# Kernel tuning notes

Hardware: AMD Instinct MI355X
Metric: run time of the kernel (lower is better)

## Reference

```python
import jax, jax.numpy as jnp
import numpy as np
import math

B, QL, KL, D, H, FF = 2, 2048, 2048, 512, 8, 2048
DH = D // H

def layernorm(x, g, b, eps=1e-5):
    m = jnp.mean(x, axis=-1, keepdims=True)
    v = jnp.mean((x - m) ** 2, axis=-1, keepdims=True)
    return (x - m) * jax.lax.rsqrt(v + eps) * g + b

def mha(x, mask, wq, bq, wk, bk, wv, bv, wo, bo, kv=None):
    # faithful port of MultiHeadAttention.forward (eval mode, dropout off)
    bs, qlen, dim = x.shape
    src = x if kv is None else kv
    def split(t):
        return t.reshape(bs, -1, H, DH).transpose(0, 2, 1, 3)  # [b,h,l,dh]
    q = split(x @ wq + bq) * (1.0 / math.sqrt(DH))
    k = split(src @ wk + bk)
    v = split(src @ wv + bv)
    scores = jnp.einsum('bhqd,bhkd->bhqk', q, k)
    m = mask[:, None, :, :] if mask.ndim == 3 else mask[:, None, None, :]
    scores = jnp.where(m == 0, -jnp.inf, scores)
    w = jax.nn.softmax(scores.astype(jnp.float32), axis=-1).astype(scores.dtype)
    ctx = jnp.einsum('bhqk,bhkd->bhqd', w, v)
    ctx = ctx.transpose(0, 2, 1, 3).reshape(bs, qlen, dim)
    return ctx @ wo + bo

def decoder_layer(tgt, memory, pos, tkpm, causal_mask, mem_mask,
                  sa, ca, l1w, l1b, l2w, l2b, n1g, n1b, n2g, n2b, n3g, n3b):
    tgt = tgt + pos
    t2 = layernorm(tgt, n1g, n1b)
    t2 = t2 * tkpm[:, :, None]
    t2 = mha(t2, causal_mask, *sa)
    tgt = tgt + t2
    t2 = layernorm(tgt, n2g, n2b)
    t2 = mha(t2, mem_mask, *ca, kv=memory)
    tgt = tgt + t2
    t2 = layernorm(tgt, n3g, n3b)
    t2 = jax.nn.relu(t2 @ l1w + l1b) @ l2w + l2b
    tgt = tgt + t2
    tgt = tgt * tkpm[:, :, None]
    return tgt

def setup_inputs() -> dict:
    key = jax.random.key(0)
    ks = jax.random.split(key, 32)
    it = iter(list(ks))
    def nrm(shape, s=0.02):
        return jax.random.normal(next(it), shape, jnp.float32) * s
    inp = {}
    inp['cfg'] = 0
    inp['tgt'] = jax.random.normal(next(it), (B, QL, D), jnp.float32)
    inp['memory'] = jax.random.normal(next(it), (B, KL, D), jnp.float32)
    inp['pos'] = jax.random.normal(next(it), (B, QL, D), jnp.float32)
    inp['causal_mask'] = jnp.broadcast_to(jnp.tril(jnp.ones((QL, QL), jnp.int32)), (B, QL, QL))
    inp['tgt_key_padding_mask'] = jnp.ones((B, QL), jnp.float32)
    mkpm = jax.random.randint(next(it), (B, KL), 0, 2).astype(jnp.int32)
    inp['memory_key_padding_mask'] = mkpm.at[:, 0].set(1)  # avoid fully-masked rows
    for p in ['sa', 'ca']:
        for w in ['q', 'k', 'v', 'o']:
            inp[f'{p}_{w}_w'] = nrm((D, D))
            inp[f'{p}_{w}_b'] = jnp.zeros((D,), jnp.float32)
    inp['lin1_w'] = nrm((D, FF)); inp['lin1_b'] = jnp.zeros((FF,), jnp.float32)
    inp['lin2_w'] = nrm((FF, D)); inp['lin2_b'] = jnp.zeros((D,), jnp.float32)
    for n in ['n1', 'n2', 'n3']:
        inp[f'{n}_g'] = jnp.ones((D,), jnp.float32)
        inp[f'{n}_b'] = jnp.zeros((D,), jnp.float32)
    return inp

def reference(cfg, tgt, memory, pos, causal_mask, tgt_key_padding_mask, memory_key_padding_mask,
              sa_q_w, sa_q_b, sa_k_w, sa_k_b, sa_v_w, sa_v_b, sa_o_w, sa_o_b,
              ca_q_w, ca_q_b, ca_k_w, ca_k_b, ca_v_w, ca_v_b, ca_o_w, ca_o_b,
              lin1_w, lin1_b, lin2_w, lin2_b,
              n1_g, n1_b, n2_g, n2_b, n3_g, n3_b):
    sa = (sa_q_w, sa_q_b, sa_k_w, sa_k_b, sa_v_w, sa_v_b, sa_o_w, sa_o_b)
    ca = (ca_q_w, ca_q_b, ca_k_w, ca_k_b, ca_v_w, ca_v_b, ca_o_w, ca_o_b)
    return decoder_layer(tgt, memory, pos, tgt_key_padding_mask, causal_mask, memory_key_padding_mask,
                         sa, ca, lin1_w, lin1_b, lin2_w, lin2_b, n1_g, n1_b, n2_g, n2_b, n3_g, n3_b)
```

## Files before the change

kernel.cpp:

```cpp
#include <hip/hip_runtime.h>
#include <hip/hip_bf16.h>
#include <stdint.h>

#define QL   2048
#define KLn  2048
#define DIM  512
#define NH   8
#define DH   64
#define NB   2
#define MROWS (NB*QL)
#define FFD  2048

typedef unsigned short u16;
typedef unsigned int u32;
typedef __attribute__((ext_vector_type(8))) short short8;
typedef __attribute__((ext_vector_type(4))) float f32x4;

__device__ __forceinline__ u16 f2b(float f){
  union { float f; u32 i; } v; v.f = f;
  u32 r = v.i + 0x7FFFu + ((v.i >> 16) & 1u);
  return (u16)(r >> 16);
}
__device__ __forceinline__ float b2f(u16 u){
  union { u32 i; float f; } v; v.i = ((u32)u) << 16; return v.f;
}
__device__ __forceinline__ u32 cvtpk(float a, float b){
  u32 r;
  asm("v_cvt_pk_bf16_f32 %0, %1, %2" : "=v"(r) : "v"(a), "v"(b));
  return r;
}

typedef __attribute__((address_space(3))) void as3void;
typedef __attribute__((address_space(1))) void as1void;
__device__ __forceinline__ void gload_lds16(const void* g, void* l){
  __builtin_amdgcn_global_load_lds((as1void*)g, (as3void*)l, 16, 0, 0);
}

#define BK 64
enum { EPI_BIAS=0, EPI_SCALEQ=1, EPI_RELU=2, EPI_RES=3, EPI_FIN=5, EPI_QKV=6, EPI_KV=7 };
#define QSCALE 0.1803368801111244f

template<int EPI>
__global__ __launch_bounds__(256, 4)
void gemm64(const u16* __restrict__ A, const u16* __restrict__ Bt,
            const float* __restrict__ bias,
            u16* __restrict__ Obf, float* __restrict__ Ores,
            const float* __restrict__ tk, float* __restrict__ fout,
            int K, int N)
{
  __shared__ __align__(16) u16 As[2][64*BK];
  __shared__ __align__(16) u16 Bs[2][64*BK];
  const int t  = threadIdx.x;
  const int l  = t & 63;
  const int lq = l & 15, lg = l >> 4;
  const int w  = t >> 6;
  const int wm = (w >> 1) * 32;
  const int wn = (w & 1) * 32;

  const int gx   = gridDim.x;
  const int nwg  = gx * gridDim.y;
  const int orig = blockIdx.x + gx * blockIdx.y;
  const int wgid = (orig & 7) * (nwg >> 3) + (orig >> 3);
  const int m0 = (wgid / gx) * 64;
  const int n0 = (wgid % gx) * 64;

  const int srow = t >> 3;
  const int scs  = t & 7;

  auto stageG = [&](u16* dA, u16* dB, int k0){
    _Pragma("unroll")
    for (int i = 0; i < 2; ++i){
      const int row = i*32 + srow;
      gload_lds16(A  + (size_t)(m0 + row)*K + k0 + ((scs ^ (row & 7)) << 3),
                  dA + row*BK + scs*8);
      gload_lds16(Bt + (size_t)(n0 + row)*K + k0 + ((scs ^ (row & 7)) << 3),
                  dB + row*BK + scs*8);
    }
  };

  int aoff[2][2], boff[2][2];
  _Pragma("unroll")
  for (int i = 0; i < 2; ++i)
    _Pragma("unroll")
    for (int kc = 0; kc < 2; ++kc){
      const int sw = (((kc*4 + lg) ^ (lq & 7)) << 3);
      aoff[i][kc] = ((wm + i*16 + lq)*BK + sw) * 2;
      boff[i][kc] = ((wn + i*16 + lq)*BK + sw) * 2;
    }

  f32x4 acc[2][2];
  _Pragma("unroll")
  for (int i=0;i<2;i++)
    _Pragma("unroll")
    for (int j=0;j<2;j++) acc[i][j] = (f32x4){0.f,0.f,0.f,0.f};

#define GBODY(BUF, KK)                                                        \
  {                                                                           \
    { const int ks = ((KK) + BK < K) ? (KK) + BK : 0;                         \
      stageG(As[(BUF)^1], Bs[(BUF)^1], ks); }                                 \
    asm volatile("s_waitcnt vmcnt(4)" ::: "memory");                          \
    __builtin_amdgcn_s_barrier();                                             \
    __builtin_amdgcn_sched_barrier(0);                                        \
    short8 af[2][2], bf[2][2];                                                \
    _Pragma("unroll")                                                         \
    for (int kc = 0; kc < 2; ++kc)                                            \
      _Pragma("unroll")                                                       \
      for (int i = 0; i < 2; ++i){                                            \
        af[i][kc] = *(const short8*)((const char*)As + (BUF)*8192 + aoff[i][kc]); \
        bf[i][kc] = *(const short8*)((const char*)Bs + (BUF)*8192 + boff[i][kc]); \
      }                                                                       \
    __builtin_amdgcn_s_barrier();                                             \
    __builtin_amdgcn_s_setprio(1);                                            \
    _Pragma("unroll")                                                         \
    for (int kc = 0; kc < 2; ++kc)                                            \
      _Pragma("unroll")                                                       \
      for (int i = 0; i < 2; ++i)                                             \
        _Pragma("unroll")                                                     \
        for (int j = 0; j < 2; ++j)                                           \
          acc[i][j] = __builtin_amdgcn_mfma_f32_16x16x32_bf16(af[i][kc], bf[j][kc], acc[i][j], 0,0,0); \
    __builtin_amdgcn_s_setprio(0);                                            \
  }

  stageG(As[0], Bs[0], 0);
  for (int k0 = 0; k0 < K; k0 += 2*BK){
    GBODY(0, k0)
    GBODY(1, k0 + BK)
  }
#undef GBODY

  _Pragma("unroll")
  for (int i=0;i<2;i++){
    _Pragma("unroll")
    for (int j=0;j<2;j++){
      _Pragma("unroll")
      for (int rr=0;rr<4;rr++){
        const int row = m0 + wm + i*16 + lg*4 + rr;
        const int col = n0 + wn + j*16 + lq;
        float v = acc[i][j][rr] + bias[col];
        if (EPI == EPI_SCALEQ) v *= QSCALE;
        if (EPI == EPI_RELU)   v = fmaxf(v, 0.f);
        if (EPI == EPI_RES)    Ores[(size_t)row*N + col] += v;
        else if (EPI == EPI_FIN){
          const size_t idx = (size_t)row*N + col;
          fout[idx] = (Ores[idx] + v) * tk[row];
        }
        else if (EPI == EPI_QKV){
          const int seg = col >> 9, c = col & 511;
          if (seg == 0)      Obf[(size_t)row*512 + c] = f2b(v * QSCALE);
          else if (seg == 1){
            const int bb = row >> 11, kv = row & 2047;
            const int hh = c >> 6,  dh = c & 63;
            Obf[(2u<<20) + ((((size_t)(bb*NH + hh) << 11) + kv) << 6) + (dh ^ ((kv & 7) << 3))] = f2b(v);
          }
          else               Obf[(4u<<20) + (size_t)row*512 + c] = f2b(v);
        }
        else if (EPI == EPI_KV){
          const int seg = col >> 9, c = col & 511;
          if (seg == 0){
            const int bb = row >> 11, kv = row & 2047;
            const int hh = c >> 6,  dh = c & 63;
            Obf[((((size_t)(bb*NH + hh) << 11) + kv) << 6) + (dh ^ ((kv & 7) << 3))] = f2b(v);
          }
          else               Obf[(2u<<20) + (size_t)row*512 + c] = f2b(v);
        }
        else                   Obf[(size_t)row*N + col] = f2b(v);
      }
    }
  }
}

template<bool CAUSAL>
__global__ __launch_bounds__(256, 4)
void attn7(const u16* __restrict__ Q, const u16* __restrict__ Kbh,
           const u16* __restrict__ Vth, const float* __restrict__ bias,
           u16* __restrict__ ctxp, float2* __restrict__ mlb)
{
  __shared__ __align__(16) u16 Kl[2][64*64];
  __shared__ __align__(16) u16 Vl[2][64*64];
  const int tid = threadIdx.x;
  const int l  = tid & 63;
  const int w  = tid >> 6;
  const int lq = l & 15, lg = l >> 4;
  const int h    = blockIdx.y;
  const int b    = blockIdx.z >> 1;
  const int half = blockIdx.z & 1;
  const int qtile = CAUSAL ? ((b & 1) ? (31 - (int)blockIdx.x) : (int)blockIdx.x)
                           : (int)blockIdx.x;
  const int q0w = qtile*64 + w*16;

  const u16* kg = Kbh + ((size_t)(b*NH + h) << 17);
  const u16* vg = Vth + ((size_t)(b*NH + h) << 17);

  short8 aq[2];
  _Pragma("unroll")
  for (int kc = 0; kc < 2; ++kc)
    aq[kc] = *(const short8*)(Q + (size_t)(b*QL + q0w + lq)*DIM + h*DH + kc*32 + lg*8);

  int koff[4][2], voff[4][2];
  _Pragma("unroll")
  for (int j = 0; j < 4; ++j)
    _Pragma("unroll")
    for (int kc = 0; kc < 2; ++kc){
      const int sw = (((kc*4 + lg) ^ (lq & 7)) << 3);
      koff[j][kc] = ((j*16 + lq)*64 + sw) * 2;
      voff[j][kc] = koff[j][kc];
    }

  f32x4 ctx[4];
  _Pragma("unroll")
  for (int d = 0; d < 4; ++d) ctx[d] = (f32x4){0.f,0.f,0.f,0.f};
  f32x4 lsum4 = (f32x4){0.f,0.f,0.f,0.f};
  float m = -INFINITY;

  const int ntiles = CAUSAL ? (qtile + 1) : (KLn >> 6);
  const int P = (ntiles > half) ? ((ntiles - half + 1) >> 1) : 0;

  auto stageA = [&](u16* dK, u16* dV, int tile){
    const u16* kgs = kg + ((size_t)tile << 12);
    const u16* vgs = vg + tile*64;
    gload_lds16(kgs + w*1024 + l*8,       dK + w*1024 + l*8);
    gload_lds16(kgs + w*1024 + 512 + l*8, dK + w*1024 + 512 + l*8);
    gload_lds16(vgs + (size_t)(w*16 +     (l>>3))*KLn + (l&7)*8, dV + w*1024 + l*8);
    gload_lds16(vgs + (size_t)(w*16 + 8 + (l>>3))*KLn + (l&7)*8, dV + w*1024 + 512 + l*8);
  };

#define ABODY(BUF, TT)                                                        \
  {                                                                           \
    f32x4 bv[4];                                                              \
    if (!CAUSAL){                                                             \
      _Pragma("unroll")                                                       \
      for (int sub = 0; sub < 4; ++sub)                                       \
        bv[sub] = *(const f32x4*)(bias + b*KLn + (TT)*64 + sub*16 + lg*4);    \
    }                                                                         \
    { const int ts = ((TT) + 2 < ntiles) ? (TT) + 2 : half;                   \
      stageA(Kl[(BUF)^1], Vl[(BUF)^1], ts); }                                 \
    if (CAUSAL) asm volatile("s_waitcnt vmcnt(4)" ::: "memory");              \
    else        asm volatile("s_waitcnt vmcnt(8)" ::: "memory");              \
    __builtin_amdgcn_s_barrier();                                             \
    __builtin_amdgcn_sched_barrier(0);                                        \
    f32x4 s[4];                                                               \
    _Pragma("unroll")                                                         \
    for (int sub = 0; sub < 4; ++sub) s[sub] = (f32x4){0.f,0.f,0.f,0.f};      \
    __builtin_amdgcn_s_setprio(1);                                            \
    _Pragma("unroll")                                                         \
    for (int sub = 0; sub < 4; ++sub)                                         \
      _Pragma("unroll")                                                       \
      for (int kc = 0; kc < 2; ++kc){                                         \
        short8 bk = *(const short8*)((const char*)Kl + (BUF)*8192 + koff[sub][kc]); \
        s[sub] = __builtin_amdgcn_mfma_f32_16x16x32_bf16(bk, aq[kc], s[sub], 0,0,0); \
      }                                                                       \
    __builtin_amdgcn_s_setprio(0);                                            \
    if (CAUSAL){                                                              \
      if ((TT)*64 + 63 > q0w){                                                \
        _Pragma("unroll")                                                     \
        for (int sub = 0; sub < 4; ++sub)                                     \
          _Pragma("unroll")                                                   \
          for (int rr = 0; rr < 4; ++rr)                                      \
            if ((TT)*64 + sub*16 + lg*4 + rr > q0w + lq) s[sub][rr] = -INFINITY; \
      }                                                                       \
    } else {                                                                  \
      _Pragma("unroll")                                                       \
      for (int sub = 0; sub < 4; ++sub) s[sub] += bv[sub];                    \
    }                                                                         \
    float mx[4];                                                              \
    _Pragma("unroll")                                                         \
    for (int sub = 0; sub < 4; ++sub)                                         \
      mx[sub] = fmaxf(fmaxf(s[sub][0], s[sub][1]), fmaxf(s[sub][2], s[sub][3])); \
    float pmax = fmaxf(fmaxf(mx[0], mx[1]), fmaxf(mx[2], mx[3]));             \
    if (!__all(pmax <= m + 8.0f)){                                            \
      pmax = fmaxf(pmax, __shfl_xor(pmax, 16));                               \
      pmax = fmaxf(pmax, __shfl_xor(pmax, 32));                               \
      const float mnew = fmaxf(m, pmax);                                      \
      const float corr = exp2f(m - mnew);                                     \
      lsum4 *= corr;                                                          \
      float corr4[4];                                                         \
      _Pragma("unroll")                                                       \
      for (int rr = 0; rr < 4; ++rr) corr4[rr] = __shfl(corr, lg*4 + rr);     \
      _Pragma("unroll")                                                       \
      for (int d = 0; d < 4; ++d)                                             \
        _Pragma("unroll")                                                     \
        for (int rr = 0; rr < 4; ++rr) ctx[d][rr] *= corr4[rr];               \
      m = mnew;                                                               \
    }                                                                         \
    u32 pk[4][2];                                                             \
    _Pragma("unroll")                                                         \
    for (int sub = 0; sub < 4; ++sub){                                        \
      float p0 = exp2f(s[sub][0] - m);                                        \
      float p1 = exp2f(s[sub][1] - m);                                        \
      float p2 = exp2f(s[sub][2] - m);                                        \
      float p3 = exp2f(s[sub][3] - m);                                        \
      lsum4 += (f32x4){p0, p1, p2, p3};                                       \
      pk[sub][0] = cvtpk(p0, p1);                                             \
      pk[sub][1] = cvtpk(p2, p3);                                             \
    }                                                                         \
    union { u32 u[4]; short8 s8; } pa0, pa1;                                  \
    pa0.u[0] = pk[0][0]; pa0.u[1] = pk[0][1]; pa0.u[2] = pk[1][0]; pa0.u[3] = pk[1][1]; \
    pa1.u[0] = pk[2][0]; pa1.u[1] = pk[2][1]; pa1.u[2] = pk[3][0]; pa1.u[3] = pk[3][1]; \
    __builtin_amdgcn_s_setprio(1);                                            \
    _Pragma("unroll")                                                         \
    for (int d0 = 0; d0 < 4; ++d0){                                           \
      short8 v0 = *(const short8*)((const char*)Vl + (BUF)*8192 + voff[d0][0]); \
      short8 v1 = *(const short8*)((const char*)Vl + (BUF)*8192 + voff[d0][1]); \
      ctx[d0] = __builtin_amdgcn_mfma_f32_16x16x32_bf16(pa0.s8, v0, ctx[d0], 0,0,0); \
      ctx[d0] = __builtin_amdgcn_mfma_f32_16x16x32_bf16(pa1.s8, v1, ctx[d0], 0,0,0); \
    }                                                                         \
    __builtin_amdgcn_s_setprio(0);                                            \
    __builtin_amdgcn_s_barrier();                                             \
  }

  if (P > 0){
    stageA(Kl[0], Vl[0], half);
    int t = half;
    for (int it = 0; it < P; it += 2){
      ABODY(0, t)
      if (it + 1 < P) ABODY(1, t + 2)
      t += 4;
    }
  }
#undef ABODY

  float hs = (lsum4[0] + lsum4[1]) + (lsum4[2] + lsum4[3]);
  hs += __shfl_xor(hs, 16);
  hs += __shfl_xor(hs, 32);
  if (lg == 0)
    mlb[((size_t)((half*NB + b)*NH + h) << 11) + q0w + lq] = make_float2(m, hs);
  u16* cp = ctxp + (size_t)half*MROWS*DIM;
  _Pragma("unroll")
  for (int d0 = 0; d0 < 4; ++d0)
    _Pragma("unroll")
    for (int rr = 0; rr < 4; ++rr)
      cp[(size_t)(b*QL + q0w + lg*4 + rr)*DIM + h*DH + d0*16 + lq] = f2b(ctx[d0][rr]);
}

__global__ __launch_bounds__(256)
void attn_merge(const u16* __restrict__ ctxp, const float2* __restrict__ mlb,
                u16* __restrict__ O)
{
  const int idx = blockIdx.x*256 + threadIdx.x;
  const int row = idx >> 7;
  const int col = (idx & 127) * 4;
  const int b = row >> 11, qr = row & 2047, h = col >> 6;
  const float2 a0 = mlb[((size_t)((      b)*NH + h) << 11) + qr];
  const float2 a1 = mlb[((size_t)((NB  + b)*NH + h) << 11) + qr];
  const float mg = fmaxf(a0.x, a1.x);
  const float w0 = exp2f(a0.x - mg), w1 = exp2f(a1.x - mg);
  const float rden = 1.f / (a0.y*w0 + a1.y*w1);
  union { uint2 v; u16 h4[4]; } c0u, c1u;
  c0u.v = *(const uint2*)&ctxp[(size_t)row*DIM + col];
  c1u.v = *(const uint2*)&ctxp[(size_t)MROWS*DIM + (size_t)row*DIM + col];
  u16 o[4];
  #pragma unroll
  for (int i = 0; i < 4; ++i)
    o[i] = f2b((b2f(c0u.h4[i])*w0 + b2f(c1u.h4[i])*w1) * rden);
  *(uint2*)&O[(size_t)row*DIM + col] = *(const uint2*)o;
}

template<int MODE>
__global__ __launch_bounds__(128)
void ln_kernel(const float* __restrict__ in0, const float* __restrict__ in1,
               const float* __restrict__ tkpm,
               const float* __restrict__ g, const float* __restrict__ bvec,
               float* __restrict__ xres, u16* __restrict__ outb)
{
  const int row = blockIdx.x;
  const int t = threadIdx.x;
  float v[4];
  #pragma unroll
  for (int i = 0; i < 4; ++i){
    const int c = t + i*128;
    float x = in0[(size_t)row*DIM + c];
    if (MODE == 0){
      x += in1[(size_t)row*DIM + c];
      xres[(size_t)row*DIM + c] = x;
    }
    v[i] = x;
  }
  float s = v[0]+v[1]+v[2]+v[3];
  #pragma unroll
  for (int off = 1; off < 64; off <<= 1) s += __shfl_xor(s, off);
  __shared__ float red[4];
  if ((t & 63) == 0) red[t >> 6] = s;
  __syncthreads();
  const float mean = (red[0] + red[1]) * (1.f/512.f);
  float q = 0.f;
  #pragma unroll
  for (int i = 0; i < 4; ++i){ const float d = v[i]-mean; q += d*d; }
  #pragma unroll
  for (int off = 1; off < 64; off <<= 1) q += __shfl_xor(q, off);
  if ((t & 63) == 0) red[2 + (t >> 6)] = q;
  __syncthreads();
  const float var = (red[2] + red[3]) * (1.f/512.f);
  const float rs = rsqrtf(var + 1e-5f);
  const float tk = (MODE == 0) ? tkpm[row] : 1.f;
  #pragma unroll
  for (int i = 0; i < 4; ++i){
    const int c = t + i*128;
    const float y = (v[i] - mean) * rs * g[c] + bvec[c];
    outb[(size_t)row*DIM + c] = f2b(y * tk);
  }
}

__global__ __launch_bounds__(256)
void prep_all(const float* w0, const float* w1, const float* w2, const float* w3,
              const float* w4, const float* w5, const float* w6, const float* w7,
              const float* __restrict__ mem, const int* __restrict__ mkpm,
              const float* saqb, const float* sakb, const float* savb,
              const float* cakb, const float* cavb,
              u16* __restrict__ wtA, u16* __restrict__ memb,
              float* __restrict__ bias, float* __restrict__ bc0,
              float* __restrict__ bc1)
{
  __shared__ float tile[32][33];
  const int id = blockIdx.x;
  const int tid = threadIdx.x;
  if (id < 2048){
    const int z = id >> 8, rem = id & 255;
    const int r0 = (rem >> 4) * 32, c0 = (rem & 15) * 32;
    const float* wp[8] = {w0,w1,w2,w3,w4,w5,w6,w7};
    const float* w = wp[z];
    u16* o = wtA + (size_t)z * 512 * 512;
    const int tx = tid & 31, ty = tid >> 5;
    #pragma unroll
    for (int i = 0; i < 4; ++i)
      tile[ty + i*8][tx] = w[(size_t)(r0 + ty + i*8)*512 + c0 + tx];
    __syncthreads();
    #pragma unroll
    for (int i = 0; i < 4; ++i)
      o[(size_t)(c0 + ty + i*8)*512 + r0 + tx] = f2b(tile[tx][ty + i*8]);
  } else if (id < 4096){
    const int i = (id - 2048)*1024 + tid*4;
    f32x4 v = *(const f32x4*)&mem[i];
    uint2 p; p.x = cvtpk(v[0], v[1]); p.y = cvtpk(v[2], v[3]);
    *(uint2*)&memb[i] = p;
  } else {
    const int j = (id - 4096)*256 + tid;
    bias[j] = mkpm[j] ? 0.f : -1e30f;
    if (j < 1536) bc0[j] = (j < 512) ? saqb[j] : (j < 1024) ? sakb[j-512] : savb[j-1024];
    if (j < 1024) bc1[j] = (j < 512) ? cakb[j] : cavb[j-512];
  }
}

__global__ __launch_bounds__(256)
void transpose_vperm(const u16* __restrict__ in, u16* __restrict__ out)
{
  __shared__ u16 tile[32][33];
  in  += (size_t)blockIdx.z * KLn * DIM;
  out += (size_t)blockIdx.z * NH * DH * KLn;
  const int tx = threadIdx.x, ty = threadIdx.y;
  const int r0 = blockIdx.y*32, c0 = blockIdx.x*32;
  #pragma unroll
  for (int i = 0; i < 4; ++i)
    tile[ty + i*8][tx] = in[(size_t)(r0 + ty + i*8)*DIM + c0 + tx];
  __syncthreads();
  const int kv = r0 + tx;
  const int s  = (kv & ~31) | (((kv>>2)&3)<<3) | (((kv>>4)&1)<<2) | (kv&3);
  #pragma unroll
  for (int i = 0; i < 4; ++i){
    const int dcol = c0 + ty + i*8;
    const int hh = dcol >> 6, dh = dcol & 63;
    const int kvpos = (s & ~63) | (((((s>>3)&7) ^ (dh&7)) << 3)) | (s & 7);
    out[((size_t)(hh*DH + dh))*KLn + kvpos] = tile[tx][ty + i*8];
  }
}

__global__ __launch_bounds__(256)
void prep_cross(const u16* __restrict__ vb, u16* __restrict__ vt,
                const float* __restrict__ l1w, u16* __restrict__ l1wt,
                const float* __restrict__ l2w, u16* __restrict__ l2wt)
{
  const int id = blockIdx.x;
  const int tid = threadIdx.x;
  const int tx = tid & 31, ty = tid >> 5;
  if (id < 2048){
    __shared__ u16 tileu[32][33];
    const int z = id >> 10, rem = id & 1023;
    const int c0 = (rem & 15) * 32, r0 = (rem >> 4) * 32;
    const u16* in = vb + (size_t)z * KLn * DIM;
    u16* out = vt + (size_t)z * NH * DH * KLn;
    #pragma unroll
    for (int i = 0; i < 4; ++i)
      tileu[ty + i*8][tx] = in[(size_t)(r0 + ty + i*8)*DIM + c0 + tx];
    __syncthreads();
    const int kv = r0 + tx;
    const int s  = (kv & ~31) | (((kv>>2)&3)<<3) | (((kv>>4)&1)<<2) | (kv&3);
    #pragma unroll
    for (int i = 0; i < 4; ++i){
      const int dcol = c0 + ty + i*8;
      const int hh = dcol >> 6, dh = dcol & 63;
      const int kvpos = (s & ~63) | (((((s>>3)&7) ^ (dh&7)) << 3)) | (s & 7);
      out[((size_t)(hh*DH + dh))*KLn + kvpos] = tileu[tx][ty + i*8];
    }
  } else {
    __shared__ float tilef[32][33];
    if (id < 3072){
      const int rem = id - 2048;
      const int c0 = (rem & 63) * 32, r0 = (rem >> 6) * 32;
      #pragma unroll
      for (int i = 0; i < 4; ++i)
        tilef[ty + i*8][tx] = l1w[(size_t)(r0 + ty + i*8)*FFD + c0 + tx];
      __syncthreads();
      #pragma unroll
      for (int i = 0; i < 4; ++i)
        l1wt[(size_t)(c0 + ty + i*8)*512 + r0 + tx] = f2b(tilef[tx][ty + i*8]);
    } else {
      const int rem = id - 3072;
      const int c0 = (rem & 15) * 32, r0 = (rem >> 4) * 32;
      #pragma unroll
      for (int i = 0; i < 4; ++i)
        tilef[ty + i*8][tx] = l2w[(size_t)(r0 + ty + i*8)*512 + c0 + tx];
      __syncthreads();
      #pragma unroll
      for (int i = 0; i < 4; ++i)
        l2wt[(size_t)(c0 + ty + i*8)*FFD + r0 + tx] = f2b(tilef[tx][ty + i*8]);
    }
  }
}

extern "C" void kernel_launch(void* const* d_in, const int* in_sizes, int n_in,
                              void* d_out, int out_size, void* d_ws, size_t ws_size,
                              hipStream_t stream)
{
  const float* tgt  = (const float*)d_in[1];
  const float* mem  = (const float*)d_in[2];
  const float* pos  = (const float*)d_in[3];
  const float* tkpm = (const float*)d_in[5];
  const int*   mkpm = (const int*)d_in[6];
  const float* saqw = (const float*)d_in[7];  const float* saqb = (const float*)d_in[8];
  const float* sakw = (const float*)d_in[9];  const float* sakb = (const float*)d_in[10];
  const float* savw = (const float*)d_in[11]; const float* savb = (const float*)d_in[12];
  const float* saow = (const float*)d_in[13]; const float* saob = (const float*)d_in[14];
  const float* caqw = (const float*)d_in[15]; const float* caqb = (const float*)d_in[16];
  const float* cakw = (const float*)d_in[17]; const float* cakb = (const float*)d_in[18];
  const float* cavw = (const float*)d_in[19]; const float* cavb = (const float*)d_in[20];
  const float* caow = (const float*)d_in[21]; const float* caob = (const float*)d_in[22];
  const float* l1w  = (const float*)d_in[23]; const float* l1b  = (const float*)d_in[24];
  const float* l2w  = (const float*)d_in[25]; const float* l2b  = (const float*)d_in[26];
  const float* n1g  = (const float*)d_in[27]; const float* n1b  = (const float*)d_in[28];
  const float* n2g  = (const float*)d_in[29]; const float* n2b  = (const float*)d_in[30];
  const float* n3g  = (const float*)d_in[31]; const float* n3b  = (const float*)d_in[32];

  if (ws_size < 58720256) return;

  char* ws = (char*)d_ws;
  float* xres = (float*)(ws);
  u16* t2n    = (u16*)(ws + (8u<<20));
  u16* qb     = (u16*)(ws + (12u<<20));
  u16* kb     = (u16*)(ws + (16u<<20));
  u16* vb     = (u16*)(ws + (20u<<20));
  u16* vt     = (u16*)(ws + (24u<<20));
  float* bias = (float*)(ws + (28u<<20));
  float* bc0  = (float*)(ws + (28u<<20) + 16384);
  float* bc1  = (float*)(ws + (28u<<20) + 24576);
  float2* mlb = (float2*)(ws + (28u<<20) + 32768);
  u16* l1wt   = (u16*)(ws + (29u<<20));
  u16* l2wt   = (u16*)(ws + (31u<<20));
  u16* memb   = (u16*)(ws + (33u<<20));
  u16* wtA    = (u16*)(ws + (37u<<20));
  u16* ctxp   = (u16*)(ws + (41u<<20));
  u16* ffh    = (u16*)(ws + (12u<<20));

  float* out = (float*)d_out;
  const int W55 = 512*512;

  prep_all<<<dim3(4112), 256, 0, stream>>>(saqw, sakw, savw, saow,
                                           caqw, cakw, cavw, caow,
                                           mem, mkpm, saqb, sakb, savb, cakb, cavb,
                                           wtA, memb, bias, bc0, bc1);
  ln_kernel<0><<<MROWS, 128, 0, stream>>>(tgt, pos, tkpm, n1g, n1b, xres, t2n);

  #define G(EP, GX) gemm64<EP><<<dim3(GX,64), 256, 0, stream>>>

  G(EPI_QKV, 24)(t2n, wtA, bc0, qb, nullptr, nullptr, nullptr, 512, 1536);
  transpose_vperm<<<dim3(DIM/32, KLn/32, NB), dim3(32,8), 0, stream>>>(vb, vt);
  attn7<true><<<dim3(QL/64, NH, NB*2), 256, 0, stream>>>(qb, kb, vt, nullptr, ctxp, mlb);
  attn_merge<<<dim3(MROWS*DIM/1024), 256, 0, stream>>>(ctxp, mlb, t2n);
  G(EPI_RES, 8)(t2n, wtA + 3*W55, saob, nullptr, xres, nullptr, nullptr, 512, 512);

  ln_kernel<1><<<MROWS, 128, 0, stream>>>(xres, nullptr, nullptr, n2g, n2b, nullptr, t2n);

  G(EPI_SCALEQ, 8)(t2n,  wtA + 4*W55, caqb, qb, nullptr, nullptr, nullptr, 512, 512);
  G(EPI_KV, 16)(memb, wtA + 5*W55, bc1, kb, nullptr, nullptr, nullptr, 512, 1024);
  prep_cross<<<dim3(4096), 256, 0, stream>>>(vb, vt, l1w, l1wt, l2w, l2wt);
  attn7<false><<<dim3(QL/64, NH, NB*2), 256, 0, stream>>>(qb, kb, vt, bias, ctxp, mlb);
  attn_merge<<<dim3(MROWS*DIM/1024), 256, 0, stream>>>(ctxp, mlb, t2n);
  G(EPI_RES, 8)(t2n, wtA + 7*W55, caob, nullptr, xres, nullptr, nullptr, 512, 512);

  ln_kernel<1><<<MROWS, 128, 0, stream>>>(xres, nullptr, nullptr, n3g, n3b, nullptr, t2n);

  G(EPI_RELU, 32)(t2n, l1wt, l1b, ffh, nullptr, nullptr, nullptr, 512, FFD);
  G(EPI_FIN, 8)(ffh, l2wt, l2b, nullptr, xres, tkpm, out, 2048, 512);

  #undef G
}
```

Before: 193.2 us.

## Process two query row groups per wave in attention to reuse K/V fragments

Each attention block now covers 128 query rows instead of 64, with every wave handling two 16-row groups that share each K and V fragment read from LDS. The LDS ring grows from 2 to 4 buffers so loads run further ahead, and occupancy drops to 2 blocks per CU. The aim is to halve LDS and global K/V traffic per query row and raise MFMA density. The cost is more registers, fewer blocks (half the grid), and coarser causal load balancing; the masked value changes from -inf to -1e30.

```diff
diff --git a/kernel.cpp b/kernel.cpp
--- a/kernel.cpp
+++ b/kernel.cpp
@@ -170,13 +170,13 @@
 }
 
 template<bool CAUSAL>
-__global__ __launch_bounds__(256, 4)
-void attn7(const u16* __restrict__ Q, const u16* __restrict__ Kbh,
+__global__ __launch_bounds__(256, 2)
+void attn8(const u16* __restrict__ Q, const u16* __restrict__ Kbh,
            const u16* __restrict__ Vth, const float* __restrict__ bias,
            u16* __restrict__ ctxp, float2* __restrict__ mlb)
 {
-  __shared__ __align__(16) u16 Kl[2][64*64];
-  __shared__ __align__(16) u16 Vl[2][64*64];
+  __shared__ __align__(16) u16 Kl[4][64*64];
+  __shared__ __align__(16) u16 Vl[4][64*64];
   const int tid = threadIdx.x;
   const int l  = tid & 63;
   const int w  = tid >> 6;
@@ -184,35 +184,37 @@
   const int h    = blockIdx.y;
   const int b    = blockIdx.z >> 1;
   const int half = blockIdx.z & 1;
-  const int qtile = CAUSAL ? ((b & 1) ? (31 - (int)blockIdx.x) : (int)blockIdx.x)
+  const int qtile = CAUSAL ? ((b & 1) ? (15 - (int)blockIdx.x) : (int)blockIdx.x)
                            : (int)blockIdx.x;
-  const int q0w = qtile*64 + w*16;
+  const int rw = qtile*128 + w*32;
 
   const u16* kg = Kbh + ((size_t)(b*NH + h) << 17);
   const u16* vg = Vth + ((size_t)(b*NH + h) << 17);
 
-  short8 aq[2];
+  short8 aq[2][2];
   _Pragma("unroll")
-  for (int kc = 0; kc < 2; ++kc)
-    aq[kc] = *(const short8*)(Q + (size_t)(b*QL + q0w + lq)*DIM + h*DH + kc*32 + lg*8);
-
-  int koff[4][2], voff[4][2];
+  for (int g = 0; g < 2; ++g)
+    _Pragma("unroll")
+    for (int kc = 0; kc < 2; ++kc)
+      aq[g][kc] = *(const short8*)(Q + (size_t)(b*QL + rw + g*16 + lq)*DIM + h*DH + kc*32 + lg*8);
+
+  int koff[4][2];
   _Pragma("unroll")
   for (int j = 0; j < 4; ++j)
     _Pragma("unroll")
-    for (int kc = 0; kc < 2; ++kc){
-      const int sw = (((kc*4 + lg) ^ (lq & 7)) << 3);
-      koff[j][kc] = ((j*16 + lq)*64 + sw) * 2;
-      voff[j][kc] = koff[j][kc];
-    }
-
-  f32x4 ctx[4];
+    for (int kc = 0; kc < 2; ++kc)
+      koff[j][kc] = ((j*16 + lq)*64 + (((kc*4 + lg) ^ (lq & 7)) << 3)) * 2;
+
+  f32x4 ctx[2][4];
   _Pragma("unroll")
-  for (int d = 0; d < 4; ++d) ctx[d] = (f32x4){0.f,0.f,0.f,0.f};
-  f32x4 lsum4 = (f32x4){0.f,0.f,0.f,0.f};
-  float m = -INFINITY;
-
-  const int ntiles = CAUSAL ? (qtile + 1) : (KLn >> 6);
+  for (int g = 0; g < 2; ++g)
+    _Pragma("unroll")
+    for (int d = 0; d < 4; ++d) ctx[g][d] = (f32x4){0.f,0.f,0.f,0.f};
+  f32x4 ls0 = (f32x4){0.f,0.f,0.f,0.f};
+  f32x4 ls1 = (f32x4){0.f,0.f,0.f,0.f};
+  float m0v = -1e30f, m1v = -1e30f;
+
+  const int ntiles = CAUSAL ? (2*qtile + 2) : (KLn >> 6);
   const int P = (ntiles > half) ? ((ntiles - half + 1) >> 1) : 0;
 
   auto stageA = [&](u16* dK, u16* dV, int tile){
@@ -224,85 +226,103 @@
     gload_lds16(vgs + (size_t)(w*16 + 8 + (l>>3))*KLn + (l&7)*8, dV + w*1024 + 512 + l*8);
   };
 
-#define ABODY(BUF, TT)                                                        \
+#define ABODY(BUF, II)                                                        \
   {                                                                           \
+    const int TT = half + 2*(II);                                             \
     f32x4 bv[4];                                                              \
     if (!CAUSAL){                                                             \
       _Pragma("unroll")                                                       \
       for (int sub = 0; sub < 4; ++sub)                                       \
-        bv[sub] = *(const f32x4*)(bias + b*KLn + (TT)*64 + sub*16 + lg*4);    \
+        bv[sub] = *(const f32x4*)(bias + b*KLn + TT*64 + sub*16 + lg*4);      \
     }                                                                         \
-    { const int ts = ((TT) + 2 < ntiles) ? (TT) + 2 : half;                   \
-      stageA(Kl[(BUF)^1], Vl[(BUF)^1], ts); }                                 \
-    if (CAUSAL) asm volatile("s_waitcnt vmcnt(4)" ::: "memory");              \
-    else        asm volatile("s_waitcnt vmcnt(8)" ::: "memory");              \
+    { const int i2 = (II) + 2;                                                \
+      const int ts = (i2 < P) ? half + 2*i2 : half;                           \
+      stageA(Kl[((BUF)+2)&3], Vl[((BUF)+2)&3], ts); }                         \
+    if (CAUSAL) asm volatile("s_waitcnt vmcnt(8)" ::: "memory");              \
+    else        asm volatile("s_waitcnt vmcnt(12)" ::: "memory");             \
     __builtin_amdgcn_s_barrier();                                             \
     __builtin_amdgcn_sched_barrier(0);                                        \
-    f32x4 s[4];                                                               \
+    f32x4 s[2][4];                                                            \
     _Pragma("unroll")                                                         \
-    for (int sub = 0; sub < 4; ++sub) s[sub] = (f32x4){0.f,0.f,0.f,0.f};      \
+    for (int g = 0; g < 2; ++g)                                               \
+      _Pragma("unroll")                                                       \
+      for (int sub = 0; sub < 4; ++sub) s[g][sub] = (f32x4){0.f,0.f,0.f,0.f}; \
     __builtin_amdgcn_s_setprio(1);                                            \
     _Pragma("unroll")                                                         \
     for (int sub = 0; sub < 4; ++sub)                                         \
       _Pragma("unroll")                                                       \
       for (int kc = 0; kc < 2; ++kc){                                         \
         short8 bk = *(const short8*)((const char*)Kl + (BUF)*8192 + koff[sub][kc]); \
-        s[sub] = __builtin_amdgcn_mfma_f32_16x16x32_bf16(bk, aq[kc], s[sub], 0,0,0); \
+        s[0][sub] = __builtin_amdgcn_mfma_f32_16x16x32_bf16(bk, aq[0][kc], s[0][sub], 0,0,0); \
+        s[1][sub] = __builtin_amdgcn_mfma_f32_16x16x32_bf16(bk, aq[1][kc], s[1][sub], 0,0,0); \
       }                                                                       \
     __builtin_amdgcn_s_setprio(0);                                            \
     if (CAUSAL){                                                              \
-      if ((TT)*64 + 63 > q0w){                                                \
+      if (TT*64 + 63 > rw){                                                   \
         _Pragma("unroll")                                                     \
-        for (int sub = 0; sub < 4; ++sub)                                     \
+        for (int g = 0; g < 2; ++g)                                           \
           _Pragma("unroll")                                                   \
-          for (int rr = 0; rr < 4; ++rr)                                      \
-            if ((TT)*64 + sub*16 + lg*4 + rr > q0w + lq) s[sub][rr] = -INFINITY; \
+          for (int sub = 0; sub < 4; ++sub)                                   \
+            _Pragma("unroll")                                                 \
+            for (int rr = 0; rr < 4; ++rr)                                    \
+              if (TT*64 + sub*16 + lg*4 + rr > rw + g*16 + lq) s[g][sub][rr] = -1e30f; \
       }                                                                       \
     } else {                                                                  \
       _Pragma("unroll")                                                       \
-      for (int sub = 0; sub < 4; ++sub) s[sub] += bv[sub];                    \
+      for (int g = 0; g < 2; ++g)                                             \
+        _Pragma("unroll")                                                     \
+        for (int sub = 0; sub < 4; ++sub) s[g][sub] += bv[sub];               \
     }                                                                         \
-    float mx[4];                                                              \
+    float px0 = s[0][0][0], px1 = s[1][0][0];                                 \
     _Pragma("unroll")                                                         \
     for (int sub = 0; sub < 4; ++sub)                                         \
-      mx[sub] = fmaxf(fmaxf(s[sub][0], s[sub][1]), fmaxf(s[sub][2], s[sub][3])); \
-    float pmax = fmaxf(fmaxf(mx[0], mx[1]), fmaxf(mx[2], mx[3]));             \
-    if (!__all(pmax <= m + 8.0f)){                                            \
-      pmax = fmaxf(pmax, __shfl_xor(pmax, 16));                               \
-      pmax = fmaxf(pmax, __shfl_xor(pmax, 32));                               \
-      const float mnew = fmaxf(m, pmax);                                      \
-      const float corr = exp2f(m - mnew);                                     \
-      lsum4 *= corr;                                                          \
-      float corr4[4];                                                         \
-      _Pragma("unroll")                                                       \
-      for (int rr = 0; rr < 4; ++rr) corr4[rr] = __shfl(corr, lg*4 + rr);     \
-      _Pragma("unroll")                                                       \
-      for (int d = 0; d < 4; ++d)                                             \
+      _Pragma("unroll")                                                       \
+      for (int rr = 0; rr < 4; ++rr){                                         \
+        px0 = fmaxf(px0, s[0][sub][rr]);                                      \
+        px1 = fmaxf(px1, s[1][sub][rr]);                                      \
+      }                                                                       \
+    if (!__all(px0 <= m0v + 8.0f && px1 <= m1v + 8.0f)){                      \
+      px0 = fmaxf(px0, __shfl_xor(px0, 16));                                  \
+      px0 = fmaxf(px0, __shfl_xor(px0, 32));                                  \
+      px1 = fmaxf(px1, __shfl_xor(px1, 16));                                  \
+      px1 = fmaxf(px1, __shfl_xor(px1, 32));                                  \
+      const float mn0 = fmaxf(m0v, px0), mn1 = fmaxf(m1v, px1);               \
+      const float c0 = exp2f(m0v - mn0), c1 = exp2f(m1v - mn1);               \
+      ls0 *= c0; ls1 *= c1;                                                   \
+      _Pragma("unroll")                                                       \
+      for (int rr = 0; rr < 4; ++rr){                                         \
+        const float b0 = __shfl(c0, lg*4 + rr), b1 = __shfl(c1, lg*4 + rr);   \
         _Pragma("unroll")                                                     \
-        for (int rr = 0; rr < 4; ++rr) ctx[d][rr] *= corr4[rr];               \
-      m = mnew;                                                               \
+        for (int d = 0; d < 4; ++d){ ctx[0][d][rr] *= b0; ctx[1][d][rr] *= b1; } \
+      }                                                                       \
+      m0v = mn0; m1v = mn1;                                                   \
     }                                                                         \
-    u32 pk[4][2];                                                             \
+    u32 pk0[4][2], pk1[4][2];                                                 \
     _Pragma("unroll")                                                         \
     for (int sub = 0; sub < 4; ++sub){                                        \
-      float p0 = exp2f(s[sub][0] - m);                                        \
-      float p1 = exp2f(s[sub][1] - m);                                        \
-      float p2 = exp2f(s[sub][2] - m);                                        \
-      float p3 = exp2f(s[sub][3] - m);                                        \
-      lsum4 += (f32x4){p0, p1, p2, p3};                                       \
-      pk[sub][0] = cvtpk(p0, p1);                                             \
-      pk[sub][1] = cvtpk(p2, p3);                                             \
+      float a0 = exp2f(s[0][sub][0] - m0v), a1 = exp2f(s[0][sub][1] - m0v);   \
+      float a2 = exp2f(s[0][sub][2] - m0v), a3 = exp2f(s[0][sub][3] - m0v);   \
+      ls0 += (f32x4){a0, a1, a2, a3};                                         \
+      pk0[sub][0] = cvtpk(a0, a1); pk0[sub][1] = cvtpk(a2, a3);               \
+      float e0 = exp2f(s[1][sub][0] - m1v), e1 = exp2f(s[1][sub][1] - m1v);   \
+      float e2 = exp2f(s[1][sub][2] - m1v), e3 = exp2f(s[1][sub][3] - m1v);   \
+      ls1 += (f32x4){e0, e1, e2, e3};                                         \
+      pk1[sub][0] = cvtpk(e0, e1); pk1[sub][1] = cvtpk(e2, e3);               \
     }                                                                         \
-    union { u32 u[4]; short8 s8; } pa0, pa1;                                  \
-    pa0.u[0] = pk[0][0]; pa0.u[1] = pk[0][1]; pa0.u[2] = pk[1][0]; pa0.u[3] = pk[1][1]; \
-    pa1.u[0] = pk[2][0]; pa1.u[1] = pk[2][1]; pa1.u[2] = pk[3][0]; pa1.u[3] = pk[3][1]; \
+    union { u32 u[4]; short8 s8; } pA0, pA1, pB0, pB1;                        \
+    pA0.u[0] = pk0[0][0]; pA0.u[1] = pk0[0][1]; pA0.u[2] = pk0[1][0]; pA0.u[3] = pk0[1][1]; \
+    pA1.u[0] = pk0[2][0]; pA1.u[1] = pk0[2][1]; pA1.u[2] = pk0[3][0]; pA1.u[3] = pk0[3][1]; \
+    pB0.u[0] = pk1[0][0]; pB0.u[1] = pk1[0][1]; pB0.u[2] = pk1[1][0]; pB0.u[3] = pk1[1][1]; \
+    pB1.u[0] = pk1[2][0]; pB1.u[1] = pk1[2][1]; pB1.u[2] = pk1[3][0]; pB1.u[3] = pk1[3][1]; \
     __builtin_amdgcn_s_setprio(1);                                            \
     _Pragma("unroll")                                                         \
     for (int d0 = 0; d0 < 4; ++d0){                                           \
-      short8 v0 = *(const short8*)((const char*)Vl + (BUF)*8192 + voff[d0][0]); \
-      short8 v1 = *(const short8*)((const char*)Vl + (BUF)*8192 + voff[d0][1]); \
-      ctx[d0] = __builtin_amdgcn_mfma_f32_16x16x32_bf16(pa0.s8, v0, ctx[d0], 0,0,0); \
-      ctx[d0] = __builtin_amdgcn_mfma_f32_16x16x32_bf16(pa1.s8, v1, ctx[d0], 0,0,0); \
+      short8 v0 = *(const short8*)((const char*)Vl + (BUF)*8192 + koff[d0][0]); \
+      short8 v1 = *(const short8*)((const char*)Vl + (BUF)*8192 + koff[d0][1]); \
+      ctx[0][d0] = __builtin_amdgcn_mfma_f32_16x16x32_bf16(pA0.s8, v0, ctx[0][d0], 0,0,0); \
+      ctx[0][d0] = __builtin_amdgcn_mfma_f32_16x16x32_bf16(pA1.s8, v1, ctx[0][d0], 0,0,0); \
+      ctx[1][d0] = __builtin_amdgcn_mfma_f32_16x16x32_bf16(pB0.s8, v0, ctx[1][d0], 0,0,0); \
+      ctx[1][d0] = __builtin_amdgcn_mfma_f32_16x16x32_bf16(pB1.s8, v1, ctx[1][d0], 0,0,0); \
     }                                                                         \
     __builtin_amdgcn_s_setprio(0);                                            \
     __builtin_amdgcn_s_barrier();                                             \
@@ -310,26 +330,34 @@
 
   if (P > 0){
     stageA(Kl[0], Vl[0], half);
-    int t = half;
-    for (int it = 0; it < P; it += 2){
-      ABODY(0, t)
-      if (it + 1 < P) ABODY(1, t + 2)
-      t += 4;
+    { const int ts1 = (1 < P) ? half + 2 : half;
+      stageA(Kl[1], Vl[1], ts1); }
+    for (int i = 0; i < P; i += 4){
+      ABODY(0, i)
+      if (i + 1 < P) ABODY(1, i + 1)
+      if (i + 2 < P) ABODY(2, i + 2)
+      if (i + 3 < P) ABODY(3, i + 3)
     }
   }
 #undef ABODY
 
-  float hs = (lsum4[0] + lsum4[1]) + (lsum4[2] + lsum4[3]);
-  hs += __shfl_xor(hs, 16);
-  hs += __shfl_xor(hs, 32);
-  if (lg == 0)
-    mlb[((size_t)((half*NB + b)*NH + h) << 11) + q0w + lq] = make_float2(m, hs);
+  float h0 = (ls0[0] + ls0[1]) + (ls0[2] + ls0[3]);
+  float h1 = (ls1[0] + ls1[1]) + (ls1[2] + ls1[3]);
+  h0 += __shfl_xor(h0, 16); h0 += __shfl_xor(h0, 32);
+  h1 += __shfl_xor(h1, 16); h1 += __shfl_xor(h1, 32);
+  if (lg == 0){
+    mlb[((size_t)((half*NB + b)*NH + h) << 11) + rw + lq]      = make_float2(m0v, h0);
+    mlb[((size_t)((half*NB + b)*NH + h) << 11) + rw + 16 + lq] = make_float2(m1v, h1);
+  }
   u16* cp = ctxp + (size_t)half*MROWS*DIM;
   _Pragma("unroll")
-  for (int d0 = 0; d0 < 4; ++d0)
-    _Pragma("unroll")
-    for (int rr = 0; rr < 4; ++rr)
-      cp[(size_t)(b*QL + q0w + lg*4 + rr)*DIM + h*DH + d0*16 + lq] = f2b(ctx[d0][rr]);
+  for (int g = 0; g < 2; ++g)
+    _Pragma("unroll")
+    for (int d0 = 0; d0 < 4; ++d0)
+      _Pragma("unroll")
+      for (int rr = 0; rr < 4; ++rr)
+        cp[(size_t)(b*QL + rw + g*16 + lg*4 + rr)*DIM + h*DH + d0*16 + lq] =
+            f2b(ctx[g][d0][rr]);
 }
 
 __global__ __launch_bounds__(256)
@@ -572,7 +600,7 @@
 
   G(EPI_QKV, 24)(t2n, wtA, bc0, qb, nullptr, nullptr, nullptr, 512, 1536);
   transpose_vperm<<<dim3(DIM/32, KLn/32, NB), dim3(32,8), 0, stream>>>(vb, vt);
-  attn7<true><<<dim3(QL/64, NH, NB*2), 256, 0, stream>>>(qb, kb, vt, nullptr, ctxp, mlb);
+  attn8<true><<<dim3(QL/128, NH, NB*2), 256, 0, stream>>>(qb, kb, vt, nullptr, ctxp, mlb);
   attn_merge<<<dim3(MROWS*DIM/1024), 256, 0, stream>>>(ctxp, mlb, t2n);
   G(EPI_RES, 8)(t2n, wtA + 3*W55, saob, nullptr, xres, nullptr, nullptr, 512, 512);
 
@@ -581,7 +609,7 @@
   G(EPI_SCALEQ, 8)(t2n,  wtA + 4*W55, caqb, qb, nullptr, nullptr, nullptr, 512, 512);
   G(EPI_KV, 16)(memb, wtA + 5*W55, bc1, kb, nullptr, nullptr, nullptr, 512, 1024);
   prep_cross<<<dim3(4096), 256, 0, stream>>>(vb, vt, l1w, l1wt, l2w, l2wt);
-  attn7<false><<<dim3(QL/64, NH, NB*2), 256, 0, stream>>>(qb, kb, vt, bias, ctxp, mlb);
+  attn8<false><<<dim3(QL/128, NH, NB*2), 256, 0, stream>>>(qb, kb, vt, bias, ctxp, mlb);
   attn_merge<<<dim3(MROWS*DIM/1024), 256, 0, stream>>>(ctxp, mlb, t2n);
   G(EPI_RES, 8)(t2n, wtA + 7*W55, caob, nullptr, xres, nullptr, nullptr, 512, 512);
 
```

Result: no change. 195.3 us (+1.1%).
